# Optimization experiments

Hardware: AMD Instinct MI355X
Metric: run time of the kernel (lower is better)

## Reference

```python
import jax, jax.numpy as jnp
import numpy as np

NUM_CLASSES = 80
MAX_DET = 100
IOU_THR = 0.5
IMG = 2048.0
N_POINTS = 262144


def setup_inputs() -> dict:
    key = jax.random.key(0)
    k1, k2, k3, k4, k5 = jax.random.split(key, 5)
    class_preds = jax.random.normal(k1, (1, N_POINTS, NUM_CLASSES), jnp.float32)
    box_preds = jax.random.normal(k2, (1, N_POINTS, 4), jnp.float32)
    centerness_preds = jax.random.normal(k3, (1, N_POINTS, 1), jnp.float32)
    points = jax.random.uniform(k4, (N_POINTS, 2), jnp.float32) * IMG
    # per-point FPN strides in {8,16,32,64,128}
    lvl = jax.random.randint(k5, (N_POINTS, 1), 0, 5).astype(jnp.float32)
    strides = 8.0 * (2.0 ** lvl)
    return {"class_preds": class_preds, "box_preds": box_preds,
            "centerness_preds": centerness_preds, "points": points,
            "strides": strides}


def box_decode(enc, pts):
    # enc = (l, t, r, b) distances from point; pts = (px, py)
    px, py = pts[..., 0], pts[..., 1]
    l, t, r, b = enc[..., 0], enc[..., 1], enc[..., 2], enc[..., 3]
    return jnp.stack([px - l, py - t, px + r, py + b], axis=-1)


def pairwise_iou(a, b):
    area_a = (a[:, 2] - a[:, 0]) * (a[:, 3] - a[:, 1])
    area_b = (b[:, 2] - b[:, 0]) * (b[:, 3] - b[:, 1])
    lt = jnp.maximum(a[:, None, :2], b[None, :, :2])
    rb = jnp.minimum(a[:, None, 2:], b[None, :, 2:])
    wh = jnp.clip(rb - lt, 0.0)
    inter = wh[..., 0] * wh[..., 1]
    return inter / (area_a[:, None] + area_b[None, :] - inter + 1e-9)


def nms_fixed(boxes, scores, iou_thr):
    # Greedy NMS over a fixed, small candidate set. Returns score-sorted
    # order and a keep mask (static shapes; suppressed entries masked).
    K = boxes.shape[0]
    order = jnp.argsort(-scores)
    b = boxes[order]
    ious = pairwise_iou(b, b)  # [K, K]
    idx = jnp.arange(K)

    def body(i, keep):
        sup = (ious[i] > iou_thr) & (idx > i) & keep[i]
        return keep & ~sup

    keep = jax.lax.fori_loop(0, K, body, jnp.ones((K,), bool))
    return order, keep


def reference(class_preds, box_preds, centerness_preds, points, strides):
    B, N, C = class_preds.shape  # B == 1 (predict path assumes single image)
    # sqrt(sigmoid(cls) * sigmoid(centerness)), flattened over (point, class)
    scores = jnp.sqrt(jax.nn.sigmoid(class_preds) * jax.nn.sigmoid(centerness_preds))
    flat = scores.reshape(B, N * C)  # [1, N*C]
    _, top_idx = jax.lax.top_k(flat, MAX_DET)  # [1, K]
    pt_idx = top_idx // C                      # point index   [1, K]
    classes = top_idx % C                      # class index   [1, K]
    # NOTE: faithful to the original torch code, which gathers the flat score
    # tensor at the *point* index (indices), not at top_indices.
    sel_scores = flat[0, pt_idx[0]]            # [K]
    sel_boxes = box_preds[0, pt_idx[0]]        # [K, 4] (l,t,r,b)
    sel_points = points[pt_idx[0]]             # [K, 2]
    sel_strides = strides[pt_idx[0]]           # [K, 1]
    dec_boxes = box_decode(sel_boxes * sel_strides, sel_points)  # [K, 4]
    order, keep = nms_fixed(dec_boxes, sel_scores, IOU_THR)
    out_boxes = jnp.where(keep[:, None], dec_boxes[order], 0.0)
    out_scores = jnp.where(keep, sel_scores[order], 0.0)
    out_classes = jnp.where(keep, classes[0][order], -1)
    return out_boxes, out_scores, out_classes
```

## Files before the change

kernel.cpp:

```cpp
#include <hip/hip_runtime.h>


#define NPTS 262144
#define NCLS 80
#define NFLAT (NPTS * NCLS)
#define NF4 (NFLAT / 4)
#define KDET 100
#define HB 1024
#define HIST_LO 0.80f
#define HIST_SCALE 5120.0f
#define BINW (1.0f / HIST_SCALE)
#define THETA0 0.94f
#define W_CAND (1.0f / (THETA0 * THETA0))
#define W_HIST (1.0f / (HIST_LO * HIST_LO))
#define MCAP 1024
#define SBUF 512
#define NB1 2560
#define NT1 256
#define UB 8
#define TT (NB1 * NT1)

__device__ __forceinline__ float s_from_w(float w) {
    return sqrtf(__builtin_amdgcn_rcpf(w));
}
__device__ __forceinline__ float sigm_p(float x) {
    return 1.0f / (1.0f + expf(-x));
}
__device__ __forceinline__ int bin_of(float s) {
    int b = (int)((s - HIST_LO) * HIST_SCALE);
    return b < 0 ? 0 : (b > HB - 1 ? HB - 1 : b);
}

__global__ __launch_bounds__(NT1) void k_score_hist(
    const float* __restrict__ cls, const float* __restrict__ cent,
    unsigned* __restrict__ hist, unsigned* __restrict__ hdr,
    float* __restrict__ cscore, unsigned* __restrict__ cidx, int cap)
{
    __shared__ unsigned sh[HB];
    __shared__ float    sbs[SBUF];
    __shared__ unsigned sbi[SBUF];
    __shared__ unsigned sbn, sbase, sbm;
    __shared__ int      lastblk;
    for (int i = threadIdx.x; i < HB; i += NT1) sh[i] = 0;
    if (threadIdx.x == 0) sbn = 0;
    __syncthreads();

    const float4* c4 = (const float4*)cls;
    int tid = blockIdx.x * NT1 + threadIdx.x;

    float4 v[UB];
    float  cb[UB];
    #pragma unroll
    for (int u = 0; u < UB; ++u) v[u] = c4[tid + u * TT];
    #pragma unroll
    for (int u = 0; u < UB; ++u) cb[u] = cent[(tid + u * TT) / 20];

    #pragma unroll
    for (int u = 0; u < UB; ++u) {
        int g = tid + u * TT;
        float f = 1.0f + __expf(-cb[u]);
        float sv[4] = {v[u].x, v[u].y, v[u].z, v[u].w};
        #pragma unroll
        for (int i = 0; i < 4; ++i) {
            float w = (1.0f + __expf(-sv[i])) * f;
            if (w <= W_HIST) {
                float s = s_from_w(w);
                atomicAdd(&sh[bin_of(s)], 1u);
                if (w <= W_CAND) {
                    unsigned pos = atomicAdd(&sbn, 1u);
                    if (pos < SBUF) { sbs[pos] = s; sbi[pos] = (unsigned)(g * 4 + i); }
                    else {
                        unsigned q = atomicAdd(&hdr[0], 1u);
                        if (q < (unsigned)cap) { cscore[q] = s; cidx[q] = (unsigned)(g * 4 + i); }
                    }
                }
            }
        }
    }
    __syncthreads();
    for (int i = threadIdx.x; i < HB; i += NT1) {
        unsigned c = sh[i];
        if (c) atomicAdd(&hist[i], c);
    }
    if (threadIdx.x == 0) {
        unsigned m = sbn < SBUF ? sbn : SBUF;
        sbm = m;
        sbase = m ? atomicAdd(&hdr[0], m) : 0u;
    }
    __syncthreads();
    for (unsigned i = threadIdx.x; i < sbm; i += NT1) {
        unsigned q = sbase + i;
        if (q < (unsigned)cap) { cscore[q] = sbs[i]; cidx[q] = sbi[i]; }
    }
    __syncthreads();
    if (threadIdx.x == 0) {
        __threadfence();
        lastblk = (atomicAdd(&hdr[3], 1u) == (unsigned)(gridDim.x - 1));
    }
    __syncthreads();
    if (!lastblk) return;
    __threadfence();
    for (int i = threadIdx.x; i < HB; i += NT1)
        sh[i] = __hip_atomic_load(&hist[i], __ATOMIC_RELAXED, __HIP_MEMORY_SCOPE_AGENT);
    __syncthreads();
    if (threadIdx.x == 0) {
        unsigned cum = 0; int T = -1;
        for (int b = HB - 1; b >= 0; --b) { cum += sh[b]; if (cum >= KDET) { T = b; break; } }
        unsigned cand = __hip_atomic_load(&hdr[0], __ATOMIC_RELAXED, __HIP_MEMORY_SCOPE_AGENT);
        int rescan;
        if (T < 0) { T = 0; rescan = 1; }
        else {
            float edgeTm1 = HIST_LO + (float)(T - 1) * BINW;
            rescan = (edgeTm1 < THETA0 + 2.0f * BINW) || (cand > (unsigned)cap);
        }
        ((int*)hdr)[2] = T;
        if (rescan) hdr[0] = 0;
        __threadfence();
        hdr[1] = (unsigned)rescan;
    }
}

__global__ __launch_bounds__(NT1) void k_rescan(
    const float* __restrict__ cls, const float* __restrict__ cent,
    unsigned* __restrict__ hdr, float* __restrict__ cscore,
    unsigned* __restrict__ cidx, int cap)
{
    if (hdr[1] == 0) return;
    int T = ((const int*)hdr)[2];
    int Tm = T > 0 ? T - 1 : 0;
    const float4* c4 = (const float4*)cls;
    int tid = blockIdx.x * NT1 + threadIdx.x;
    float4 v[UB];
    float  cb[UB];
    #pragma unroll
    for (int u = 0; u < UB; ++u) v[u] = c4[tid + u * TT];
    #pragma unroll
    for (int u = 0; u < UB; ++u) cb[u] = cent[(tid + u * TT) / 20];
    #pragma unroll
    for (int u = 0; u < UB; ++u) {
        int g = tid + u * TT;
        float f = 1.0f + __expf(-cb[u]);
        float sv[4] = {v[u].x, v[u].y, v[u].z, v[u].w};
        #pragma unroll
        for (int i = 0; i < 4; ++i) {
            float w = (1.0f + __expf(-sv[i])) * f;
            if (w <= W_HIST) {
                float s = s_from_w(w);
                if (bin_of(s) >= Tm) {
                    unsigned pos = atomicAdd(&hdr[0], 1u);
                    if (pos < (unsigned)cap) { cscore[pos] = s; cidx[pos] = (unsigned)(g * 4 + i); }
                }
            }
        }
    }
}

__global__ __launch_bounds__(256) void k_finalize(
    const float* __restrict__ cls, const float* __restrict__ cent,
    const float* __restrict__ boxp, const float* __restrict__ pts,
    const float* __restrict__ strd,
    const unsigned* __restrict__ hdr, const float* __restrict__ cscore,
    const unsigned* __restrict__ cidx, int cap, float* __restrict__ out)
{
    __shared__ float    ss[MCAP];
    __shared__ unsigned si[MCAP];
    __shared__ float    ps[MCAP];
    __shared__ unsigned mcnt;
    __shared__ float    tks[KDET];
    __shared__ unsigned tkj[KDET];
    __shared__ float sel_s[KDET];
    __shared__ int   sel_c[KDET];
    __shared__ float sel_b[KDET][4];
    __shared__ int   ordv[KDET];
    __shared__ float bs[KDET][4];
    __shared__ float sso[KDET];
    __shared__ int   cso[KDET];
    __shared__ unsigned char keepA[KDET];
    __shared__ float ioum[KDET * KDET];

    int T = ((const int*)hdr)[2];
    int Tm = T > 0 ? T - 1 : 0;
    unsigned n = hdr[0]; if (n > (unsigned)cap) n = (unsigned)cap;
    if (threadIdx.x == 0) mcnt = 0;
    __syncthreads();

    for (unsigned i = threadIdx.x; i < n; i += 256) {
        float s = cscore[i];
        if (bin_of(s) >= Tm) {
            unsigned p = atomicAdd(&mcnt, 1u);
            if (p < MCAP) { ss[p] = s; si[p] = cidx[i]; }
        }
    }
    __syncthreads();
    unsigned M = mcnt < MCAP ? mcnt : MCAP;

    for (unsigned m = threadIdx.x; m < M; m += 256) {
        unsigned j = si[m];
        ps[m] = sqrtf(sigm_p(cls[j]) * sigm_p(cent[j / (unsigned)NCLS]));
    }
    if (threadIdx.x < KDET) { tks[threadIdx.x] = -1.0f; tkj[threadIdx.x] = 0u; }
    __syncthreads();

    for (unsigned m = threadIdx.x; m < M; m += 256) {
        float sm = ps[m]; unsigned jm = si[m];
        int rank = 0;
        for (unsigned q = 0; q < M; ++q) {
            float sq = ps[q]; unsigned jq = si[q];
            if (sq > sm || (sq == sm && jq < jm)) ++rank;
        }
        if (rank < KDET) { tks[rank] = sm; tkj[rank] = jm; }
    }
    __syncthreads();

    if (threadIdx.x < KDET) {
        int k = threadIdx.x;
        unsigned j = tkj[k];
        unsigned pt = j / (unsigned)NCLS;
        sel_c[k] = (int)(j % (unsigned)NCLS);
        sel_s[k] = sqrtf(sigm_p(cls[pt]) * sigm_p(cent[pt / (unsigned)NCLS]));
        float l = boxp[pt * 4 + 0], tt = boxp[pt * 4 + 1];
        float r = boxp[pt * 4 + 2], bb = boxp[pt * 4 + 3];
        float st = strd[pt];
        float px = pts[pt * 2 + 0], py = pts[pt * 2 + 1];
        sel_b[k][0] = __fsub_rn(px, __fmul_rn(l,  st));
        sel_b[k][1] = __fsub_rn(py, __fmul_rn(tt, st));
        sel_b[k][2] = __fadd_rn(px, __fmul_rn(r,  st));
        sel_b[k][3] = __fadd_rn(py, __fmul_rn(bb, st));
    }
    __syncthreads();

    if (threadIdx.x < KDET) {
        int k = threadIdx.x; float sk = sel_s[k]; int rank = 0;
        for (int j = 0; j < KDET; ++j) {
            float sj = sel_s[j];
            if (sj > sk || (sj == sk && j < k)) ++rank;
        }
        ordv[rank] = k;
    }
    __syncthreads();
    if (threadIdx.x < KDET) {
        int i = threadIdx.x, o = ordv[i];
        sso[i] = sel_s[o]; cso[i] = sel_c[o];
        bs[i][0] = sel_b[o][0]; bs[i][1] = sel_b[o][1];
        bs[i][2] = sel_b[o][2]; bs[i][3] = sel_b[o][3];
        keepA[i] = 1;
    }
    __syncthreads();

    for (int t = threadIdx.x; t < KDET * KDET; t += 256) {
        int i = t / KDET, j = t % KDET;
        float ax1 = bs[i][0], ay1 = bs[i][1], ax2 = bs[i][2], ay2 = bs[i][3];
        float bx1 = bs[j][0], by1 = bs[j][1], bx2 = bs[j][2], by2 = bs[j][3];
        float areaA = (ax2 - ax1) * (ay2 - ay1);
        float areaB = (bx2 - bx1) * (by2 - by1);
        float lx = fmaxf(ax1, bx1), ly = fmaxf(ay1, by1);
        float rx = fminf(ax2, bx2), ry = fminf(ay2, by2);
        float w = fmaxf(rx - lx, 0.0f), h = fmaxf(ry - ly, 0.0f);
        float inter = w * h;
        ioum[t] = inter / (areaA + areaB - inter + 1e-9f);
    }
    __syncthreads();

    if (threadIdx.x < 64) {
        int L = threadIdx.x;
        int k0 = 1, k1 = 1;
        #pragma unroll 1
        for (int i = 0; i < KDET; ++i) {
            int owner = (i < 64) ? i : (i - 64);
            int flag  = (i < 64) ? k0 : k1;
            int keep_i = __shfl(flag, owner, 64);
            if (keep_i) {
                if (L > i && ioum[i * KDET + L] > 0.5f) k0 = 0;
                int j2 = L + 64;
                if (j2 > i && j2 < KDET && ioum[i * KDET + j2] > 0.5f) k1 = 0;
            }
        }
        keepA[L] = (unsigned char)k0;
        if (L + 64 < KDET) keepA[L + 64] = (unsigned char)k1;
    }
    __syncthreads();

    if (threadIdx.x < KDET) {
        int i = threadIdx.x;
        bool kp = keepA[i] != 0;
        out[i * 4 + 0] = kp ? bs[i][0] : 0.0f;
        out[i * 4 + 1] = kp ? bs[i][1] : 0.0f;
        out[i * 4 + 2] = kp ? bs[i][2] : 0.0f;
        out[i * 4 + 3] = kp ? bs[i][3] : 0.0f;
        out[4 * KDET + i] = kp ? sso[i] : 0.0f;
        out[5 * KDET + i] = kp ? (float)cso[i] : -1.0f;
    }
}

extern "C" void kernel_launch(void* const* d_in, const int* in_sizes, int n_in,
                              void* d_out, int out_size, void* d_ws, size_t ws_size,
                              hipStream_t stream)
{
    const float* cls  = (const float*)d_in[0];
    const float* boxp = (const float*)d_in[1];
    const float* cent = (const float*)d_in[2];
    const float* pts  = (const float*)d_in[3];
    const float* strd = (const float*)d_in[4];
    float* out = (float*)d_out;

    char* ws = (char*)d_ws;
    unsigned* hdr  = (unsigned*)ws;
    unsigned* hist = (unsigned*)(ws + 16);
    size_t capS = ws_size > 4360 ? (ws_size - 4352) / 8 : 64;
    int cap = (int)(capS > 32768 ? 32768 : capS);
    float*    cscore = (float*)(ws + 4352);
    unsigned* cidx   = (unsigned*)(ws + 4352 + (size_t)cap * 4);

    hipMemsetAsync(d_ws, 0, 4112, stream);
    hipLaunchKernelGGL(k_score_hist, dim3(NB1), dim3(NT1), 0, stream,
                       cls, cent, hist, hdr, cscore, cidx, cap);
    hipLaunchKernelGGL(k_rescan, dim3(NB1), dim3(NT1), 0, stream,
                       cls, cent, hdr, cscore, cidx, cap);
    hipLaunchKernelGGL(k_finalize, dim3(1), dim3(256), 0, stream,
                       cls, cent, boxp, pts, strd, hdr, cscore, cidx, cap, out);
}
```

Baseline: 291.8 us.

## Drop rescan kernel, fold rare fallback rescan into finalize, shrink histogram

Removes the separate full-grid rescan kernel launch and moves the fallback full scan into the single-block finalize kernel, where it runs only when the histogram threshold check fails. The histogram is narrowed to 256 bins over [0.9, 1.0], and the shared staging buffer is reduced. The centerness loads are now issued before the class loads, with a compiler barrier after them. This saves one kernel launch and its early-exit grid. The cost is that the rare fallback path becomes a very slow single-block scan of all 21M scores.

```diff
diff --git a/kernel.cpp b/kernel.cpp
--- a/kernel.cpp
+++ b/kernel.cpp
@@ -6,15 +6,15 @@
 #define NFLAT (NPTS * NCLS)
 #define NF4 (NFLAT / 4)
 #define KDET 100
-#define HB 1024
-#define HIST_LO 0.80f
-#define HIST_SCALE 5120.0f
+#define HB 256
+#define HIST_LO 0.90f
+#define HIST_SCALE 2560.0f
 #define BINW (1.0f / HIST_SCALE)
 #define THETA0 0.94f
 #define W_CAND (1.0f / (THETA0 * THETA0))
 #define W_HIST (1.0f / (HIST_LO * HIST_LO))
 #define MCAP 1024
-#define SBUF 512
+#define SBUF 128
 #define NB1 2560
 #define NT1 256
 #define UB 8
@@ -31,7 +31,7 @@
     return b < 0 ? 0 : (b > HB - 1 ? HB - 1 : b);
 }
 
-__global__ __launch_bounds__(NT1) void k_score_hist(
+__global__ __launch_bounds__(NT1) void k_scan(
     const float* __restrict__ cls, const float* __restrict__ cent,
     unsigned* __restrict__ hist, unsigned* __restrict__ hdr,
     float* __restrict__ cscore, unsigned* __restrict__ cidx, int cap)
@@ -48,12 +48,13 @@
     const float4* c4 = (const float4*)cls;
     int tid = blockIdx.x * NT1 + threadIdx.x;
 
+    float  cb[UB];
     float4 v[UB];
-    float  cb[UB];
+    #pragma unroll
+    for (int u = 0; u < UB; ++u) cb[u] = cent[(tid + u * TT) / 20];
     #pragma unroll
     for (int u = 0; u < UB; ++u) v[u] = c4[tid + u * TT];
-    #pragma unroll
-    for (int u = 0; u < UB; ++u) cb[u] = cent[(tid + u * TT) / 20];
+    asm volatile("" ::: "memory");
 
     #pragma unroll
     for (int u = 0; u < UB; ++u) {
@@ -67,11 +68,12 @@
                 float s = s_from_w(w);
                 atomicAdd(&sh[bin_of(s)], 1u);
                 if (w <= W_CAND) {
+                    unsigned gi = (unsigned)(g * 4 + i);
                     unsigned pos = atomicAdd(&sbn, 1u);
-                    if (pos < SBUF) { sbs[pos] = s; sbi[pos] = (unsigned)(g * 4 + i); }
+                    if (pos < SBUF) { sbs[pos] = s; sbi[pos] = gi; }
                     else {
                         unsigned q = atomicAdd(&hdr[0], 1u);
-                        if (q < (unsigned)cap) { cscore[q] = s; cidx[q] = (unsigned)(g * 4 + i); }
+                        if (q < (unsigned)cap) { cscore[q] = s; cidx[q] = gi; }
                     }
                 }
             }
@@ -114,44 +116,8 @@
             rescan = (edgeTm1 < THETA0 + 2.0f * BINW) || (cand > (unsigned)cap);
         }
         ((int*)hdr)[2] = T;
-        if (rescan) hdr[0] = 0;
         __threadfence();
         hdr[1] = (unsigned)rescan;
-    }
-}
-
-__global__ __launch_bounds__(NT1) void k_rescan(
-    const float* __restrict__ cls, const float* __restrict__ cent,
-    unsigned* __restrict__ hdr, float* __restrict__ cscore,
-    unsigned* __restrict__ cidx, int cap)
-{
-    if (hdr[1] == 0) return;
-    int T = ((const int*)hdr)[2];
-    int Tm = T > 0 ? T - 1 : 0;
-    const float4* c4 = (const float4*)cls;
-    int tid = blockIdx.x * NT1 + threadIdx.x;
-    float4 v[UB];
-    float  cb[UB];
-    #pragma unroll
-    for (int u = 0; u < UB; ++u) v[u] = c4[tid + u * TT];
-    #pragma unroll
-    for (int u = 0; u < UB; ++u) cb[u] = cent[(tid + u * TT) / 20];
-    #pragma unroll
-    for (int u = 0; u < UB; ++u) {
-        int g = tid + u * TT;
-        float f = 1.0f + __expf(-cb[u]);
-        float sv[4] = {v[u].x, v[u].y, v[u].z, v[u].w};
-        #pragma unroll
-        for (int i = 0; i < 4; ++i) {
-            float w = (1.0f + __expf(-sv[i])) * f;
-            if (w <= W_HIST) {
-                float s = s_from_w(w);
-                if (bin_of(s) >= Tm) {
-                    unsigned pos = atomicAdd(&hdr[0], 1u);
-                    if (pos < (unsigned)cap) { cscore[pos] = s; cidx[pos] = (unsigned)(g * 4 + i); }
-                }
-            }
-        }
     }
 }
 
@@ -180,15 +146,35 @@
 
     int T = ((const int*)hdr)[2];
     int Tm = T > 0 ? T - 1 : 0;
-    unsigned n = hdr[0]; if (n > (unsigned)cap) n = (unsigned)cap;
     if (threadIdx.x == 0) mcnt = 0;
     __syncthreads();
 
-    for (unsigned i = threadIdx.x; i < n; i += 256) {
-        float s = cscore[i];
-        if (bin_of(s) >= Tm) {
-            unsigned p = atomicAdd(&mcnt, 1u);
-            if (p < MCAP) { ss[p] = s; si[p] = cidx[i]; }
+    if (hdr[1]) {
+        const float4* c4 = (const float4*)cls;
+        for (int g = threadIdx.x; g < NF4; g += 256) {
+            float4 vv = c4[g];
+            float f = 1.0f + __expf(-cent[g / 20]);
+            float sv[4] = {vv.x, vv.y, vv.z, vv.w};
+            #pragma unroll
+            for (int i = 0; i < 4; ++i) {
+                float w = (1.0f + __expf(-sv[i])) * f;
+                if (w <= W_HIST) {
+                    float s = s_from_w(w);
+                    if (bin_of(s) >= Tm) {
+                        unsigned p = atomicAdd(&mcnt, 1u);
+                        if (p < MCAP) { ss[p] = s; si[p] = (unsigned)(g * 4 + i); }
+                    }
+                }
+            }
+        }
+    } else {
+        unsigned n = hdr[0]; if (n > (unsigned)cap) n = (unsigned)cap;
+        for (unsigned i = threadIdx.x; i < n; i += 256) {
+            float s = cscore[i];
+            if (bin_of(s) >= Tm) {
+                unsigned p = atomicAdd(&mcnt, 1u);
+                if (p < MCAP) { ss[p] = s; si[p] = cidx[i]; }
+            }
         }
     }
     __syncthreads();
@@ -306,16 +292,14 @@
     char* ws = (char*)d_ws;
     unsigned* hdr  = (unsigned*)ws;
     unsigned* hist = (unsigned*)(ws + 16);
-    size_t capS = ws_size > 4360 ? (ws_size - 4352) / 8 : 64;
+    size_t capS = ws_size > 2056 ? (ws_size - 2048) / 8 : 64;
     int cap = (int)(capS > 32768 ? 32768 : capS);
-    float*    cscore = (float*)(ws + 4352);
-    unsigned* cidx   = (unsigned*)(ws + 4352 + (size_t)cap * 4);
-
-    hipMemsetAsync(d_ws, 0, 4112, stream);
-    hipLaunchKernelGGL(k_score_hist, dim3(NB1), dim3(NT1), 0, stream,
+    float*    cscore = (float*)(ws + 2048);
+    unsigned* cidx   = (unsigned*)(ws + 2048 + (size_t)cap * 4);
+
+    hipMemsetAsync(d_ws, 0, 2048, stream);
+    hipLaunchKernelGGL(k_scan, dim3(NB1), dim3(NT1), 0, stream,
                        cls, cent, hist, hdr, cscore, cidx, cap);
-    hipLaunchKernelGGL(k_rescan, dim3(NB1), dim3(NT1), 0, stream,
-                       cls, cent, hdr, cscore, cidx, cap);
     hipLaunchKernelGGL(k_finalize, dim3(1), dim3(256), 0, stream,
                        cls, cent, boxp, pts, strd, hdr, cscore, cidx, cap, out);
 }
```

Measured after the change: 285.2 us. 2.3% less time.
